# Optimization experiments

Measured on AMD Instinct MI355X. Metric: run time of the kernel, lower is better.

## Reference

```python
import jax, jax.numpy as jnp
import numpy as np

VOCAB = 50257
D_MODEL = 1024
RANK = 64
V1, V2 = 225, 224   # ceil(sqrt(vocab)), ceil(vocab/v1)
D1, D2 = 32, 32     # ceil(sqrt(d_model)), ceil(d_model/d1)
B, L = 4, 4096


def setup_inputs() -> dict:
    key = jax.random.key(0)
    ks = jax.random.split(key, 4)
    input_ids = jax.random.randint(ks[0], (B, L), 0, VOCAB, dtype=jnp.int32)
    core1_q = jax.random.randint(ks[1], (V1, 1, RANK, D1), -128, 128, dtype=jnp.int32).astype(jnp.int8)
    core2_q = jax.random.randint(ks[2], (V2, RANK, 1, D2), -128, 128, dtype=jnp.int32).astype(jnp.int8)
    phase_shift = jax.random.normal(ks[3], (RANK,), dtype=jnp.float32) * 0.02
    return {
        "input_ids": input_ids,
        "core1_q": core1_q,
        "core1_scale": jnp.float32(0.01),
        "core1_zp": jnp.float32(0.0),
        "core2_q": core2_q,
        "core2_scale": jnp.float32(0.01),
        "core2_zp": jnp.float32(0.0),
        "phase_shift": phase_shift,
    }


def reference(input_ids, core1_q, core1_scale, core1_zp, core2_q, core2_scale, core2_zp, phase_shift):
    # token index -> (row in core1, row in core2)
    idx1 = jnp.clip(input_ids // V2, 0, V1 - 1)  # [B, L]
    idx2 = jnp.clip(input_ids % V2, 0, V2 - 1)   # [B, L]

    # gather int8 rows first, then dequantize: (q - zp) * scale (same math as
    # dequantizing full cores then gathering, but avoids touching unused rows)
    c1 = (core1_q[idx1, 0].astype(jnp.float32) - core1_zp) * core1_scale     # [B, L, R, D1]
    c2 = (core2_q[idx2, :, 0].astype(jnp.float32) - core2_zp) * core2_scale  # [B, L, R, D2]

    # phase modulation on core1 along the rank axis
    c1 = c1 * jnp.cos(phase_shift)[None, None, :, None]

    # per-token rank contraction: [B,L,D1,D2] -> [B,L,D1*D2] -> slice d_model
    out = jnp.einsum('blrd,blrf->bldf', c1, c2).reshape(B, L, D1 * D2)
    return out[:, :, :D_MODEL]
```

## Files before the change

kernel.cpp:

```cpp
#include <hip/hip_runtime.h>
#include <hip/hip_bf16.h>
#include <math.h>

#define V1N   225
#define V2N   224
#define RANK  64
#define DDIM  32
#define ROWE  (RANK*DDIM)

typedef __bf16  bf16x8 __attribute__((ext_vector_type(8)));
typedef float  f32x16 __attribute__((ext_vector_type(16)));
typedef float  f32x4  __attribute__((ext_vector_type(4)));
typedef int    i32x4  __attribute__((ext_vector_type(4)));

__global__ __launch_bounds__(256) void prep_tables(
    const int* __restrict__ c1q, const int* __restrict__ c2q,
    const float* __restrict__ s1p, const float* __restrict__ z1p,
    const float* __restrict__ s2p, const float* __restrict__ z2p,
    const float* __restrict__ phase,
    __bf16* __restrict__ t1, __bf16* __restrict__ t2)
{
    __shared__ float cosv[RANK];
    __shared__ float lds[4][64 * 33];

    int t = threadIdx.x;
    if (t < RANK) cosv[t] = cosf(phase[t]);
    __syncthreads();

    int w    = t >> 6;
    int lane = t & 63;
    int v    = blockIdx.x * 4 + w;
    if (v >= V1N + V2N) return;

    bool is1 = (v < V1N);
    const int* src; __bf16* dst; float sc, zp;
    if (is1) { src = c1q + (size_t)v * ROWE;            dst = t1 + (size_t)v * ROWE;  sc = *s1p; zp = *z1p; }
    else     { int u = v - V1N; src = c2q + (size_t)u * ROWE; dst = t2 + (size_t)u * ROWE; sc = *s2p; zp = *z2p; }

    float* L = lds[w];
    #pragma unroll
    for (int p = 0; p < 4; ++p) {
        i32x4 q0 = reinterpret_cast<const i32x4*>(src)[p * 128 + lane * 2];
        i32x4 q1 = reinterpret_cast<const i32x4*>(src)[p * 128 + lane * 2 + 1];
        #pragma unroll
        for (int j = 0; j < 8; ++j) {
            int e = p * 512 + lane * 8 + j;
            int q = (j < 4) ? q0[j & 3] : q1[j & 3];
            float val = ((float)q - zp) * sc;
            if (is1) val *= cosv[e >> 5];
            L[(e >> 5) * 33 + (e & 31)] = val;
        }
    }
    #pragma unroll
    for (int h = 0; h < 4; ++h) {
        int d   = lane >> 1;
        int rr0 = (lane & 1) * 8;
        bf16x8 o8;
        #pragma unroll
        for (int j = 0; j < 8; ++j) {
            int r = h * 16 + rr0 + j;
            o8[j] = (__bf16)L[r * 33 + d];
        }
        *reinterpret_cast<bf16x8*>(dst + h * 512 + lane * 8) = o8;
    }
}

__global__ __launch_bounds__(256) void tt_main(
    const int* __restrict__ ids,
    const __bf16* __restrict__ t1, const __bf16* __restrict__ t2,
    float* __restrict__ out, int n_tok)
{
    __shared__ float tile[4][2][32 * 33];

    int w    = threadIdx.x >> 6;
    int lane = threadIdx.x & 63;
    int m = lane & 31;
    int g = lane >> 5;
    int tok0 = ((blockIdx.x << 2) + w) * 2;
    int tok1 = tok0 + 1;
    bool act0 = (tok0 < n_tok);
    bool act1 = (tok1 < n_tok);

    bf16x8 a0[4], b0[4], a1[4], b1[4];

    if (act0) {
        unsigned id = (unsigned)ids[tok0];
        unsigned i1 = id / 224u; if (i1 > (unsigned)(V1N - 1)) i1 = V1N - 1;
        unsigned i2 = id % 224u;
        const __bf16* ab = t2 + (size_t)i2 * ROWE + m * 16 + g * 8;
        const __bf16* bb = t1 + (size_t)i1 * ROWE + m * 16 + g * 8;
        #pragma unroll
        for (int s = 0; s < 4; ++s) {
            a0[s] = *reinterpret_cast<const bf16x8*>(ab + s * 512);
            b0[s] = *reinterpret_cast<const bf16x8*>(bb + s * 512);
        }
    }
    if (act1) {
        unsigned id = (unsigned)ids[tok1];
        unsigned i1 = id / 224u; if (i1 > (unsigned)(V1N - 1)) i1 = V1N - 1;
        unsigned i2 = id % 224u;
        const __bf16* ab = t2 + (size_t)i2 * ROWE + m * 16 + g * 8;
        const __bf16* bb = t1 + (size_t)i1 * ROWE + m * 16 + g * 8;
        #pragma unroll
        for (int s = 0; s < 4; ++s) {
            a1[s] = *reinterpret_cast<const bf16x8*>(ab + s * 512);
            b1[s] = *reinterpret_cast<const bf16x8*>(bb + s * 512);
        }
    }

    if (act0) {
        f32x16 acc;
        #pragma unroll
        for (int i = 0; i < 16; ++i) acc[i] = 0.0f;
        #pragma unroll
        for (int s = 0; s < 4; ++s)
            acc = __builtin_amdgcn_mfma_f32_32x32x16_bf16(a0[s], b0[s], acc, 0, 0, 0);

        float* tp = tile[w][0];
        #pragma unroll
        for (int q = 0; q < 4; ++q)
            #pragma unroll
            for (int j = 0; j < 4; ++j)
                tp[m * 33 + 8 * q + 4 * g + j] = acc[4 * q + j];

        float* o = out + (size_t)tok0 * 1024;
        #pragma unroll
        for (int p = 0; p < 4; ++p) {
            int d1 = p * 8 + (lane >> 3);
            int d2 = (lane & 7) * 4;
            f32x4 v = { tp[d1 * 33 + d2 + 0], tp[d1 * 33 + d2 + 1],
                        tp[d1 * 33 + d2 + 2], tp[d1 * 33 + d2 + 3] };
            *reinterpret_cast<f32x4*>(o + p * 256 + lane * 4) = v;
        }
    }

    if (act1) {
        f32x16 acc;
        #pragma unroll
        for (int i = 0; i < 16; ++i) acc[i] = 0.0f;
        #pragma unroll
        for (int s = 0; s < 4; ++s)
            acc = __builtin_amdgcn_mfma_f32_32x32x16_bf16(a1[s], b1[s], acc, 0, 0, 0);

        float* tp = tile[w][1];
        #pragma unroll
        for (int q = 0; q < 4; ++q)
            #pragma unroll
            for (int j = 0; j < 4; ++j)
                tp[m * 33 + 8 * q + 4 * g + j] = acc[4 * q + j];

        float* o = out + (size_t)tok1 * 1024;
        #pragma unroll
        for (int p = 0; p < 4; ++p) {
            int d1 = p * 8 + (lane >> 3);
            int d2 = (lane & 7) * 4;
            f32x4 v = { tp[d1 * 33 + d2 + 0], tp[d1 * 33 + d2 + 1],
                        tp[d1 * 33 + d2 + 2], tp[d1 * 33 + d2 + 3] };
            *reinterpret_cast<f32x4*>(o + p * 256 + lane * 4) = v;
        }
    }
}

__global__ __launch_bounds__(256) void tt_fused(
    const int* __restrict__ ids,
    const int* __restrict__ c1q, const int* __restrict__ c2q,
    const float* __restrict__ s1p, const float* __restrict__ z1p,
    const float* __restrict__ s2p, const float* __restrict__ z2p,
    const float* __restrict__ phase,
    float* __restrict__ out, int n_tok)
{
    __shared__ float cosv[RANK];
    if (threadIdx.x < RANK) cosv[threadIdx.x] = cosf(phase[threadIdx.x]);
    __syncthreads();

    int wave = (blockIdx.x << 2) + (threadIdx.x >> 6);
    if (wave >= n_tok) return;
    int lane = threadIdx.x & 63;
    int m = lane & 31;
    int g = lane >> 5;

    float s1 = *s1p, z1 = *z1p, s2 = *s2p, z2 = *z2p;

    unsigned id = (unsigned)ids[wave];
    unsigned i1 = id / 224u; if (i1 > (unsigned)(V1N - 1)) i1 = V1N - 1;
    unsigned i2 = id % 224u;

    const int* a_src = c2q + (size_t)i2 * ROWE + m;
    const int* b_src = c1q + (size_t)i1 * ROWE + m;

    f32x16 acc;
    #pragma unroll
    for (int i = 0; i < 16; ++i) acc[i] = 0.0f;

    #pragma unroll
    for (int s = 0; s < 4; ++s) {
        bf16x8 a, b;
        #pragma unroll
        for (int j = 0; j < 8; ++j) {
            int r = s * 16 + g * 8 + j;
            a[j] = (__bf16)((((float)a_src[r * 32]) - z2) * s2);
            b[j] = (__bf16)((((float)b_src[r * 32]) - z1) * s1 * cosv[r]);
        }
        acc = __builtin_amdgcn_mfma_f32_32x32x16_bf16(a, b, acc, 0, 0, 0);
    }

    float* o = out + (size_t)wave * 1024 + m * 32 + g * 4;
    #pragma unroll
    for (int q = 0; q < 4; ++q) {
        f32x4 v = { acc[4 * q + 0], acc[4 * q + 1], acc[4 * q + 2], acc[4 * q + 3] };
        *reinterpret_cast<f32x4*>(o + 8 * q) = v;
    }
}

extern "C" void kernel_launch(void* const* d_in, const int* in_sizes, int n_in,
                              void* d_out, int out_size, void* d_ws, size_t ws_size,
                              hipStream_t stream) {
    const int*   ids = (const int*)d_in[0];
    const int*   c1q = (const int*)d_in[1];
    const float* s1  = (const float*)d_in[2];
    const float* z1  = (const float*)d_in[3];
    const int*   c2q = (const int*)d_in[4];
    const float* s2  = (const float*)d_in[5];
    const float* z2  = (const float*)d_in[6];
    const float* ph  = (const float*)d_in[7];
    float* out = (float*)d_out;

    int n_tok = in_sizes[0];
    int grid  = (n_tok + 7) / 8;

    size_t need = (size_t)(V1N + V2N) * ROWE * sizeof(__bf16);
    if (ws_size >= need) {
        __bf16* t1 = (__bf16*)d_ws;
        __bf16* t2 = t1 + (size_t)V1N * ROWE;
        prep_tables<<<(V1N + V2N + 3) / 4, 256, 0, stream>>>(c1q, c2q, s1, z1, s2, z2, ph, t1, t2);
        tt_main<<<grid, 256, 0, stream>>>(ids, t1, t2, out, n_tok);
    } else {
        int fgrid = (n_tok + 3) / 4;
        tt_fused<<<fgrid, 256, 0, stream>>>(ids, c1q, c2q, s1, z1, s2, z2, ph, out, n_tok);
    }
}
```

Before: 26.07 us.

## Process eight tokens per wave with software-pipelined gathers of table rows

Each wave in the main kernel now handles eight consecutive tokens instead of two. It computes all row offsets up front and prefetches the next token's bf16 table rows while running the MFMA and store for the current one, ping-ponging between two LDS tiles. The goal is to overlap gather latency with compute and output writes and to cut per-block launch overhead. In exchange the grid has fewer blocks and registers go up, which may lower occupancy and parallelism.

```diff
diff --git a/kernel.cpp b/kernel.cpp
--- a/kernel.cpp
+++ b/kernel.cpp
@@ -7,6 +7,7 @@
 #define RANK  64
 #define DDIM  32
 #define ROWE  (RANK*DDIM)
+#define TPW   8
 
 typedef __bf16  bf16x8 __attribute__((ext_vector_type(8)));
 typedef float  f32x16 __attribute__((ext_vector_type(16)));
@@ -76,87 +77,70 @@
     int lane = threadIdx.x & 63;
     int m = lane & 31;
     int g = lane >> 5;
-    int tok0 = ((blockIdx.x << 2) + w) * 2;
-    int tok1 = tok0 + 1;
-    bool act0 = (tok0 < n_tok);
-    bool act1 = (tok1 < n_tok);
-
-    bf16x8 a0[4], b0[4], a1[4], b1[4];
-
-    if (act0) {
-        unsigned id = (unsigned)ids[tok0];
+    int t0 = (blockIdx.x * 4 + w) * TPW;
+    if (t0 >= n_tok) return;
+
+    int aoff[TPW], boff[TPW];
+    #pragma unroll
+    for (int i = 0; i < TPW; ++i) {
+        int t = t0 + i;
+        unsigned id = (unsigned)ids[t < n_tok ? t : (n_tok - 1)];
         unsigned i1 = id / 224u; if (i1 > (unsigned)(V1N - 1)) i1 = V1N - 1;
         unsigned i2 = id % 224u;
-        const __bf16* ab = t2 + (size_t)i2 * ROWE + m * 16 + g * 8;
-        const __bf16* bb = t1 + (size_t)i1 * ROWE + m * 16 + g * 8;
-        #pragma unroll
-        for (int s = 0; s < 4; ++s) {
-            a0[s] = *reinterpret_cast<const bf16x8*>(ab + s * 512);
-            b0[s] = *reinterpret_cast<const bf16x8*>(bb + s * 512);
-        }
-    }
-    if (act1) {
-        unsigned id = (unsigned)ids[tok1];
-        unsigned i1 = id / 224u; if (i1 > (unsigned)(V1N - 1)) i1 = V1N - 1;
-        unsigned i2 = id % 224u;
-        const __bf16* ab = t2 + (size_t)i2 * ROWE + m * 16 + g * 8;
-        const __bf16* bb = t1 + (size_t)i1 * ROWE + m * 16 + g * 8;
-        #pragma unroll
-        for (int s = 0; s < 4; ++s) {
-            a1[s] = *reinterpret_cast<const bf16x8*>(ab + s * 512);
-            b1[s] = *reinterpret_cast<const bf16x8*>(bb + s * 512);
-        }
-    }
-
-    if (act0) {
+        aoff[i] = (int)(i2 * ROWE);
+        boff[i] = (int)(i1 * ROWE);
+    }
+    const __bf16* abase = t2 + m * 16 + g * 8;
+    const __bf16* bbase = t1 + m * 16 + g * 8;
+
+    bf16x8 aC[4], bC[4];
+    #pragma unroll
+    for (int s = 0; s < 4; ++s) {
+        aC[s] = *reinterpret_cast<const bf16x8*>(abase + aoff[0] + s * 512);
+        bC[s] = *reinterpret_cast<const bf16x8*>(bbase + boff[0] + s * 512);
+    }
+
+    #pragma unroll
+    for (int k = 0; k < TPW; ++k) {
+        bf16x8 aN[4], bN[4];
+        if (k + 1 < TPW) {
+            #pragma unroll
+            for (int s = 0; s < 4; ++s) {
+                aN[s] = *reinterpret_cast<const bf16x8*>(abase + aoff[k + 1] + s * 512);
+                bN[s] = *reinterpret_cast<const bf16x8*>(bbase + boff[k + 1] + s * 512);
+            }
+        }
+
         f32x16 acc;
         #pragma unroll
         for (int i = 0; i < 16; ++i) acc[i] = 0.0f;
         #pragma unroll
         for (int s = 0; s < 4; ++s)
-            acc = __builtin_amdgcn_mfma_f32_32x32x16_bf16(a0[s], b0[s], acc, 0, 0, 0);
-
-        float* tp = tile[w][0];
+            acc = __builtin_amdgcn_mfma_f32_32x32x16_bf16(aC[s], bC[s], acc, 0, 0, 0);
+
+        float* tp = tile[w][k & 1];
         #pragma unroll
         for (int q = 0; q < 4; ++q)
             #pragma unroll
             for (int j = 0; j < 4; ++j)
                 tp[m * 33 + 8 * q + 4 * g + j] = acc[4 * q + j];
 
-        float* o = out + (size_t)tok0 * 1024;
-        #pragma unroll
-        for (int p = 0; p < 4; ++p) {
-            int d1 = p * 8 + (lane >> 3);
-            int d2 = (lane & 7) * 4;
-            f32x4 v = { tp[d1 * 33 + d2 + 0], tp[d1 * 33 + d2 + 1],
-                        tp[d1 * 33 + d2 + 2], tp[d1 * 33 + d2 + 3] };
-            *reinterpret_cast<f32x4*>(o + p * 256 + lane * 4) = v;
-        }
-    }
-
-    if (act1) {
-        f32x16 acc;
-        #pragma unroll
-        for (int i = 0; i < 16; ++i) acc[i] = 0.0f;
-        #pragma unroll
-        for (int s = 0; s < 4; ++s)
-            acc = __builtin_amdgcn_mfma_f32_32x32x16_bf16(a1[s], b1[s], acc, 0, 0, 0);
-
-        float* tp = tile[w][1];
-        #pragma unroll
-        for (int q = 0; q < 4; ++q)
-            #pragma unroll
-            for (int j = 0; j < 4; ++j)
-                tp[m * 33 + 8 * q + 4 * g + j] = acc[4 * q + j];
-
-        float* o = out + (size_t)tok1 * 1024;
-        #pragma unroll
-        for (int p = 0; p < 4; ++p) {
-            int d1 = p * 8 + (lane >> 3);
-            int d2 = (lane & 7) * 4;
-            f32x4 v = { tp[d1 * 33 + d2 + 0], tp[d1 * 33 + d2 + 1],
-                        tp[d1 * 33 + d2 + 2], tp[d1 * 33 + d2 + 3] };
-            *reinterpret_cast<f32x4*>(o + p * 256 + lane * 4) = v;
+        int tok = t0 + k;
+        if (tok < n_tok) {
+            float* o = out + (size_t)tok * 1024;
+            #pragma unroll
+            for (int p = 0; p < 4; ++p) {
+                int d1 = p * 8 + (lane >> 3);
+                int d2 = (lane & 7) * 4;
+                f32x4 v = { tp[d1 * 33 + d2 + 0], tp[d1 * 33 + d2 + 1],
+                            tp[d1 * 33 + d2 + 2], tp[d1 * 33 + d2 + 3] };
+                *reinterpret_cast<f32x4*>(o + p * 256 + lane * 4) = v;
+            }
+        }
+
+        if (k + 1 < TPW) {
+            #pragma unroll
+            for (int s = 0; s < 4; ++s) { aC[s] = aN[s]; bC[s] = bN[s]; }
         }
     }
 }
@@ -226,7 +210,7 @@
     float* out = (float*)d_out;
 
     int n_tok = in_sizes[0];
-    int grid  = (n_tok + 7) / 8;
+    int grid  = (n_tok + 4 * TPW - 1) / (4 * TPW);
 
     size_t need = (size_t)(V1N + V2N) * ROWE * sizeof(__bf16);
     if (ws_size >= need) {
```

Measured after the change: 25.94 us. No clear change (-0.5%).
